# Kernel tuning notes

Measured on AMD Instinct MI355X. Metric: run time of the kernel, lower is better.

The kernel has to match this reference:

```python
import jax, jax.numpy as jnp
import numpy as np

B, S, T = 128, 1024, 512
VOCAB, E, HE, HD, ATT = 1000, 128, 64, 66, 32


def setup_inputs() -> dict:
    key = jax.random.key(0)
    ks = jax.random.split(key, 14)
    p = lambda k, shape: (jax.random.normal(k, shape, dtype=jnp.float32) * 0.05)
    return {
        'x': jax.random.randint(ks[0], (B, S), 0, VOCAB, dtype=jnp.int32),
        'c': jax.random.normal(ks[1], (B, T), dtype=jnp.float32),
        'emb': p(ks[2], (VOCAB, E)),
        'enc_Wih': p(ks[3], (4 * HE, E)),
        'enc_Whh': p(ks[4], (4 * HE, HE)),
        'enc_b': p(ks[5], (4 * HE,)),
        'att_fc_W': p(ks[6], (HE, E)),
        'att_fc_b': p(ks[7], (HE,)),
        'att_w_W': p(ks[8], (ATT, HE)),
        'att_w_b': p(ks[9], (ATT,)),
        'dec_Wih': p(ks[10], (4 * HD, ATT)),
        'dec_Whh': p(ks[11], (4 * HD, HD)),
        'dec_b': p(ks[12], (4 * HD,)),
        'fin_W': p(ks[13], (E, HD)),
        'fin_b': jnp.zeros((E,), dtype=jnp.float32),
    }


def _lstm_seq(xs, W_ih, W_hh, b, H):
    # xs: [B, S, in]; PyTorch gate order i, f, g, o
    bsz = xs.shape[0]
    gx = jnp.einsum('bsi,gi->bsg', xs, W_ih) + b  # [B,S,4H]

    def step(carry, g_t):
        h, c = carry
        g = g_t + h @ W_hh.T
        i, f, gg, o = jnp.split(g, 4, axis=-1)
        c = jax.nn.sigmoid(f) * c + jax.nn.sigmoid(i) * jnp.tanh(gg)
        h = jax.nn.sigmoid(o) * jnp.tanh(c)
        return (h, c), h

    h0 = jnp.zeros((bsz, H), xs.dtype)
    (_, _), hs = jax.lax.scan(step, (h0, h0), jnp.swapaxes(gx, 0, 1))
    return jnp.swapaxes(hs, 0, 1)  # [B,S,H]


def reference(x, c, emb, enc_Wih, enc_Whh, enc_b, att_fc_W, att_fc_b,
              att_w_W, att_w_b, dec_Wih, dec_Whh, dec_b, fin_W, fin_b):
    # encoder: embed + LSTM, returns full sequence of hidden states [B,S,64]
    enc = _lstm_seq(emb[x], enc_Wih, enc_Whh, enc_b, HE)
    bsz, steps = x.shape[0], c.shape[1]
    # initial decoder input: embedding of token 0, broadcast over batch
    x0 = jnp.broadcast_to(emb[0], (bsz, E))
    h0 = jnp.zeros((bsz, HD), enc.dtype)

    def step(carry, _):
        xemb, h, cc = carry
        # attend(a=xemb, A=enc)
        a = xemb @ att_fc_W.T + att_fc_b                     # [B,64]
        A = a[:, None, :] * enc                              # [B,S,64]
        alpha = jax.nn.softmax(
            jnp.tanh(jnp.einsum('bse,ae->bsa', A, att_w_W) + att_w_b),
            axis=-1)                                         # [B,S,32]
        beta = alpha.sum(axis=1)                             # [B,32]
        # decoder LSTM cell (one timestep)
        g = beta @ dec_Wih.T + h @ dec_Whh.T + dec_b
        i, f, gg, o = jnp.split(g, 4, axis=-1)
        cc = jax.nn.sigmoid(f) * cc + jax.nn.sigmoid(i) * jnp.tanh(gg)
        h = jax.nn.sigmoid(o) * jnp.tanh(cc)
        xemb = h @ fin_W.T + fin_b                           # feed back via final_fc
        return (xemb, h, cc), h

    _, hs = jax.lax.scan(step, (x0, h0, h0), None, length=steps)
    return jnp.swapaxes(hs, 0, 1)  # [B,T,66]
```

## Files before the change

### kernel.cpp

```cpp
#include <hip/hip_runtime.h>
#include <hip/hip_bf16.h>

#define kB 128
#define kS 1024
#define kT 512
#define kV 1000
#define kE 128
#define kHE 64
#define kHD 66
#define kATT 32
#define kGE 256
#define kGD 264

typedef __attribute__((ext_vector_type(4))) float f32x4;
typedef __attribute__((ext_vector_type(8))) short bf16x8;
typedef __attribute__((ext_vector_type(8))) unsigned short u16x8;

__device__ __forceinline__ unsigned short f2bf(float f) {
  unsigned int u = __builtin_bit_cast(unsigned int, f);
  u += 0x7FFFu + ((u >> 16) & 1u);
  return (unsigned short)(u >> 16);
}
__device__ __forceinline__ float rcp_(float x) { return __builtin_amdgcn_rcpf(x); }
__device__ __forceinline__ float fsig(float x)  { return rcp_(1.0f + __expf(-x)); }
__device__ __forceinline__ float ftanh(float x) { return 1.0f - 2.0f * rcp_(1.0f + __expf(2.0f * x)); }
__device__ __forceinline__ float fexp2(float z) {
#if __has_builtin(__builtin_amdgcn_exp2f)
  return __builtin_amdgcn_exp2f(z);
#else
  return __expf(z * 0.6931471805599453f);
#endif
}
__device__ __forceinline__ const unsigned short* launder_us(const unsigned short* p) {
  asm volatile("" : "+s"(p));
  return p;
}
__device__ __forceinline__ float dpp_red16(float v) {
  int x = __builtin_bit_cast(int, v);
  v += __builtin_bit_cast(float, __builtin_amdgcn_update_dpp(0, x, 0xB1, 0xf, 0xf, true));
  x = __builtin_bit_cast(int, v);
  v += __builtin_bit_cast(float, __builtin_amdgcn_update_dpp(0, x, 0x4E, 0xf, 0xf, true));
  x = __builtin_bit_cast(int, v);
  v += __builtin_bit_cast(float, __builtin_amdgcn_update_dpp(0, x, 0x124, 0xf, 0xf, true));
  x = __builtin_bit_cast(int, v);
  v += __builtin_bit_cast(float, __builtin_amdgcn_update_dpp(0, x, 0x128, 0xf, 0xf, true));
  return v;
}
#define DPPB(v, ctrl) __builtin_bit_cast(float, __builtin_amdgcn_update_dpp(0, __builtin_bit_cast(int, (v)), (ctrl), 0xf, 0xf, true))

__global__ __launch_bounds__(256) void prep_kernel(
    const float* __restrict__ emb, const float* __restrict__ enc_Wih,
    const float* __restrict__ enc_b, const float* __restrict__ enc_Whh,
    const float* __restrict__ att_fc_W, const float* __restrict__ att_fc_b,
    const float* __restrict__ att_w_W,
    const float* __restrict__ fin_W, const float* __restrict__ fin_b,
    const float* __restrict__ dec_Wih, const float* __restrict__ dec_Whh,
    const float* __restrict__ dec_b,
    float* __restrict__ embW, unsigned short* __restrict__ decF,
    unsigned short* __restrict__ encF, unsigned short* __restrict__ afF,
    float* __restrict__ wregF, float* __restrict__ dbias,
    float* __restrict__ wh64, float* __restrict__ wh65,
    float* __restrict__ abias, float* __restrict__ ainit) {
  int bid = blockIdx.x, tid = threadIdx.x;
  if (bid < kV) {
    float acc = enc_b[tid];
    const float* er = emb + bid * kE;
    const float* wr = enc_Wih + tid * kE;
    for (int e = 0; e < kE; ++e) acc += er[e] * wr[e];
    embW[bid * kGE + tid] = acc;
  } else if (bid == kV) {
    for (int i = tid; i < 17 * 3 * 64 * 8; i += 256) {
      int jj = i & 7, lane = (i >> 3) & 63, ts = i >> 9;
      int tile = ts / 3, ks = ts - tile * 3;
      int jp = tile * 16 + (lane & 15);
      int cell = jp >> 2, gate = jp & 3;
      int k = ks * 32 + ((lane >> 4) << 3) + jj;
      float v = 0.f;
      if (cell < kHD) {
        int j = gate * kHD + cell;
        if (k < 32) v = dec_Wih[j * kATT + k];
        else v = dec_Whh[j * kHD + (k - 32)];
      }
      decF[i] = f2bf(v);
    }
  } else if (bid == kV + 1) {
    for (int i = tid; i < 16 * 2 * 64 * 8; i += 256) {
      int jj = i & 7, lane = (i >> 3) & 63, ts = i >> 9;
      int tile = ts >> 1, ks = ts & 1;
      int j = tile * 16 + (lane & 15);
      int k = ks * 32 + ((lane >> 4) << 3) + jj;
      encF[i] = f2bf(enc_Whh[j * kHE + k]);
    }
  } else if (bid == kV + 2) {
    for (int i = tid; i < 4 * 3 * 64 * 8; i += 256) {
      int jj = i & 7, lane = (i >> 3) & 63, ts = i >> 9;
      int tile = ts / 3, ks = ts - tile * 3;
      int aidx = tile * 16 + (lane & 15);
      int m = ks * 32 + ((lane >> 4) << 3) + jj;
      float v = 0.f;
      if (m < kHD)
        for (int e = 0; e < kE; ++e) v += att_fc_W[aidx * kE + e] * fin_W[e * kHD + m];
      afF[i] = f2bf(v);
    }
  } else if (bid == kV + 3) {
    for (int i = tid; i < 8 * 64 * 4; i += 256) {
      int c = i & 3, lane = (i >> 2) & 63, jq = i >> 8;
      int half = jq & 1, kc = (jq >> 1) & 1, mt = jq >> 2;
      wregF[i] = att_w_W[(mt * 16 + (lane & 15)) * kHE + kc * 32 + ((lane >> 4) << 3) + half * 4 + c];
    }
  } else if (bid == kV + 4) {
    for (int jp = tid; jp < kGD; jp += 256) {
      int cell = jp >> 2, gate = jp & 3;
      int j = gate * kHD + cell;
      float s = 0.f;
      for (int m = 0; m < kATT; ++m) s += dec_Wih[j * kATT + m];
      dbias[jp] = dec_b[j] + 32.0f * s;
      wh64[jp] = dec_Whh[j * kHD + 64];
      wh65[jp] = dec_Whh[j * kHD + 65];
    }
  } else {
    if (tid < kHE) {
      float acc = att_fc_b[tid];
      for (int e = 0; e < kE; ++e) acc += att_fc_W[tid * kE + e] * fin_b[e];
      abias[tid] = acc;
    } else if (tid < 2 * kHE) {
      int a = tid - kHE;
      float acc = att_fc_b[a];
      for (int e = 0; e < kE; ++e) acc += emb[e] * att_fc_W[a * kE + e];
      ainit[a] = acc;
    }
  }
}

__global__ __launch_bounds__(256)
__attribute__((amdgpu_waves_per_eu(1, 1)))
void enc_kernel(
    const int* __restrict__ x, const float* __restrict__ embW,
    const unsigned short* __restrict__ encF, float* __restrict__ out) {
  __shared__ struct __align__(16) {
    unsigned short xe[64];
    float gbuf[kGE];
    int toks[kS];
  } sm;
  const int b = blockIdx.x, t = threadIdx.x, lane = t & 63, wv = t >> 6;

  for (int i = t; i < kS; i += 256) sm.toks[i] = x[b * kS + i];
  if (t < 64) sm.xe[t] = 0;

  u16x8 eQ[4][2];
  #pragma unroll
  for (int q = 0; q < 4; ++q)
    #pragma unroll
    for (int ks = 0; ks < 2; ++ks)
      eQ[q][ks] = *(const u16x8*)&encF[(((wv * 4 + q) * 2 + ks) * 64 + lane) * 8];
  __syncthreads();

  float gx0 = 0, gx1 = 0, gx2 = 0, gx3 = 0;
  if (lane < 16) {
    int tok = sm.toks[0];
    gx0 = embW[tok * kGE + wv * 64 + 0 + lane];
    gx1 = embW[tok * kGE + wv * 64 + 16 + lane];
    gx2 = embW[tok * kGE + wv * 64 + 32 + lane];
    gx3 = embW[tok * kGE + wv * 64 + 48 + lane];
  }
  float cE = 0.0f;
  unsigned short* eg = (unsigned short*)(out + (size_t)b * (kT * kHD));

  for (int s = 0; s < kS; ++s) {
    union { u16x8 u; bf16x8 v; } xa0, xa1;
    xa0.u = *(const u16x8*)&sm.xe[(lane >> 4) << 3];
    xa1.u = *(const u16x8*)&sm.xe[32 + ((lane >> 4) << 3)];
    float gn0 = 0, gn1 = 0, gn2 = 0, gn3 = 0;
    int tokn = sm.toks[(s + 1 < kS) ? (s + 1) : s];
    if (lane < 16) {
      gn0 = embW[tokn * kGE + wv * 64 + 0 + lane];
      gn1 = embW[tokn * kGE + wv * 64 + 16 + lane];
      gn2 = embW[tokn * kGE + wv * 64 + 32 + lane];
      gn3 = embW[tokn * kGE + wv * 64 + 48 + lane];
    }
    f32x4 z = {0.f, 0.f, 0.f, 0.f};
    f32x4 a0 = __builtin_amdgcn_mfma_f32_16x16x32_bf16(xa0.v, eQ[0][0], z, 0, 0, 0);
    a0 = __builtin_amdgcn_mfma_f32_16x16x32_bf16(xa1.v, eQ[0][1], a0, 0, 0, 0);
    f32x4 a1 = __builtin_amdgcn_mfma_f32_16x16x32_bf16(xa0.v, eQ[1][0], z, 0, 0, 0);
    a1 = __builtin_amdgcn_mfma_f32_16x16x32_bf16(xa1.v, eQ[1][1], a1, 0, 0, 0);
    f32x4 a2 = __builtin_amdgcn_mfma_f32_16x16x32_bf16(xa0.v, eQ[2][0], z, 0, 0, 0);
    a2 = __builtin_amdgcn_mfma_f32_16x16x32_bf16(xa1.v, eQ[2][1], a2, 0, 0, 0);
    f32x4 a3 = __builtin_amdgcn_mfma_f32_16x16x32_bf16(xa0.v, eQ[3][0], z, 0, 0, 0);
    a3 = __builtin_amdgcn_mfma_f32_16x16x32_bf16(xa1.v, eQ[3][1], a3, 0, 0, 0);
    if (lane < 16) {
      sm.gbuf[wv * 64 + 0 + lane]  = a0[0] + gx0;
      sm.gbuf[wv * 64 + 16 + lane] = a1[0] + gx1;
      sm.gbuf[wv * 64 + 32 + lane] = a2[0] + gx2;
      sm.gbuf[wv * 64 + 48 + lane] = a3[0] + gx3;
    }
    __syncthreads();
    if (t < 64) {
      float gi = sm.gbuf[t], gf = sm.gbuf[64 + t], gg = sm.gbuf[128 + t], go = sm.gbuf[192 + t];
      cE = fsig(gf) * cE + fsig(gi) * ftanh(gg);
      float h = fsig(go) * ftanh(cE);
      unsigned short hb = f2bf(h);
      sm.xe[t] = hb;
      eg[s * 64 + ((((t >> 3) ^ (s & 7)) << 3) | (t & 7))] = hb;
    }
    __syncthreads();
    gx0 = gn0; gx1 = gn1; gx2 = gn2; gx3 = gn3;
  }
}

struct __align__(16) DSm {
  unsigned short enc[kS * kHE];
  float wregL[8 * 64 * 4];
  float dbL[kGD];
  float wh64L[kGD];
  float wh65L[kGD];
  float absL[64];
  float aa[64];
  float beta[32];
  unsigned short xv[2][160];
  float hh2[2][2];
};

union U8 { u16x8 u; bf16x8 v; };

__global__ __launch_bounds__(512, 2)
void dec_kernel(
    const float* __restrict__ att_w_b,
    const unsigned short* __restrict__ decF, const unsigned short* __restrict__ afF,
    const float* __restrict__ wregF_ws, const float* __restrict__ dbias_ws,
    const float* __restrict__ wh64_ws, const float* __restrict__ wh65_ws,
    const float* __restrict__ abias_ws, const float* __restrict__ ainit_ws,
    float* __restrict__ out) {
  __shared__ DSm sm;
  const int b = blockIdx.x, t = threadIdx.x, lane = t & 63, wv = t >> 6;
  const int lr = lane & 15, g = lane >> 4;

  {
    const u16x8* src = (const u16x8*)(out + (size_t)b * (kT * kHD));
    u16x8* dst = (u16x8*)sm.enc;
    #pragma unroll
    for (int i = 0; i < 16; ++i) dst[t + i * 512] = src[t + i * 512];
  }
  ((f32x4*)sm.wregL)[t] = ((const f32x4*)wregF_ws)[t];
  for (int i = t; i < kGD; i += 512) {
    sm.dbL[i] = dbias_ws[i];
    sm.wh64L[i] = wh64_ws[i];
    sm.wh65L[i] = wh65_ws[i];
  }
  if (t < 64) { sm.absL[t] = abias_ws[t]; sm.aa[t] = ainit_ws[t]; }
  if (t < 32) sm.beta[t] = 0.f;
  for (int i = t; i < 320; i += 512) ((unsigned short*)sm.xv)[i] = 0;
  if (t < 4) ((float*)sm.hh2)[t] = 0.f;

  const float bw0 = att_w_b[lr];
  const float bw1 = att_w_b[16 + lr];
  U8 aQ[3];
  if (wv < 4) {
    #pragma unroll
    for (int ks = 0; ks < 3; ++ks)
      aQ[ks].u = *(const u16x8*)&afF[((wv * 3 + ks) * 64 + lane) * 8];
  }
  float cDa = 0.0f, cDb = 0.0f, cDc = 0.0f;
  __syncthreads();

  const int sbase = wv * 128;
  const int tileA = wv, tileB = wv + 8;
  const bool has3 = (wv == 7);

  for (int step = 0; step < kT; ++step) {
    const int cb = step & 1, nb = cb ^ 1;
    U8 qa[3], qb[3], qc[3];
    {
      const f32x4* aap = (const f32x4*)sm.aa;
      const f32x4* wrl = (const f32x4*)sm.wregL;
      bf16x8 af[2][2];
      #pragma unroll
      for (int kc = 0; kc < 2; ++kc) {
        f32x4 a0v = aap[kc * 8 + g * 2];
        f32x4 a1v = aap[kc * 8 + g * 2 + 1];
        #pragma unroll
        for (int mt = 0; mt < 2; ++mt) {
          f32x4 w0 = wrl[((mt * 2 + kc) * 2 + 0) * 64 + lane];
          f32x4 w1 = wrl[((mt * 2 + kc) * 2 + 1) * 64 + lane];
          union { bf16x8 v; __hip_bfloat162 h2[4]; } tmp;
          tmp.h2[0] = __float22bfloat162_rn(make_float2(w0.x * a0v.x, w0.y * a0v.y));
          tmp.h2[1] = __float22bfloat162_rn(make_float2(w0.z * a0v.z, w0.w * a0v.w));
          tmp.h2[2] = __float22bfloat162_rn(make_float2(w1.x * a1v.x, w1.y * a1v.y));
          tmp.h2[3] = __float22bfloat162_rn(make_float2(w1.z * a1v.z, w1.w * a1v.w));
          af[mt][kc] = tmp.v;
        }
      }
      f32x4 wc0 = {bw0, bw0, bw0, bw0};
      f32x4 wc1 = {bw1, bw1, bw1, bw1};
      float betaAcc[2] = {0.f, 0.f};
      float amax = 0.0f;
      #pragma unroll
      for (int nt = 0; nt < 8; ++nt) {
        int s = sbase + nt * 16 + lr;
        int sw = s & 7;
        U8 e0, e1;
        e0.u = *(const u16x8*)&sm.enc[s * kHE + ((g ^ sw) << 3)];
        e1.u = *(const u16x8*)&sm.enc[s * kHE + (((4 + g) ^ sw) << 3)];
        f32x4 acc0 = __builtin_amdgcn_mfma_f32_16x16x32_bf16(e0.v, af[0][0], wc0, 0, 0, 0);
        acc0 = __builtin_amdgcn_mfma_f32_16x16x32_bf16(e1.v, af[0][1], acc0, 0, 0, 0);
        f32x4 acc1 = __builtin_amdgcn_mfma_f32_16x16x32_bf16(e0.v, af[1][0], wc1, 0, 0, 0);
        acc1 = __builtin_amdgcn_mfma_f32_16x16x32_bf16(e1.v, af[1][1], acc1, 0, 0, 0);
        float u0[4], u1[4];
        #pragma unroll
        for (int r = 0; r < 4; ++r) {
          float x0 = acc0[r], x1 = acc1[r];
          amax = fmaxf(amax, fmaxf(__builtin_fabsf(x0), __builtin_fabsf(x1)));
          u0[r] = fexp2(x0 * __builtin_fmaf(x0 * x0, -0.48089835f, 1.44269504f));
          u1[r] = fexp2(x1 * __builtin_fmaf(x1 * x1, -0.48089835f, 1.44269504f));
        }
        #pragma unroll
        for (int r = 0; r < 4; ++r) {
          float invd = rcp_(dpp_red16(u0[r] + u1[r]));
          betaAcc[0] += u0[r] * invd;
          betaAcc[1] += u1[r] * invd;
        }
      }
      if (__builtin_expect(__any(amax > 0.35f), 0)) {
        betaAcc[0] = 0.f; betaAcc[1] = 0.f;
        for (int nt = 0; nt < 8; ++nt) {
          int s = sbase + nt * 16 + lr;
          int sw = s & 7;
          U8 e0, e1;
          e0.u = *(const u16x8*)&sm.enc[s * kHE + ((g ^ sw) << 3)];
          e1.u = *(const u16x8*)&sm.enc[s * kHE + (((4 + g) ^ sw) << 3)];
          f32x4 acc0 = __builtin_amdgcn_mfma_f32_16x16x32_bf16(e0.v, af[0][0], wc0, 0, 0, 0);
          acc0 = __builtin_amdgcn_mfma_f32_16x16x32_bf16(e1.v, af[0][1], acc0, 0, 0, 0);
          f32x4 acc1 = __builtin_amdgcn_mfma_f32_16x16x32_bf16(e0.v, af[1][0], wc1, 0, 0, 0);
          acc1 = __builtin_amdgcn_mfma_f32_16x16x32_bf16(e1.v, af[1][1], acc1, 0, 0, 0);
          float u0[4], u1[4];
          for (int r = 0; r < 4; ++r) {
            u0[r] = __expf(tanhf(acc0[r]));
            u1[r] = __expf(tanhf(acc1[r]));
          }
          for (int r = 0; r < 4; ++r) {
            float invd = rcp_(dpp_red16(u0[r] + u1[r]));
            betaAcc[0] += u0[r] * invd;
            betaAcc[1] += u1[r] * invd;
          }
        }
      }
      {
        const unsigned short* dFp = launder_us(decF);
        #pragma unroll
        for (int ks = 0; ks < 3; ++ks) {
          qa[ks].u = *(const u16x8*)&dFp[((tileA * 3 + ks) * 64 + lane) * 8];
          qb[ks].u = *(const u16x8*)&dFp[((tileB * 3 + ks) * 64 + lane) * 8];
        }
        if (has3) {
          #pragma unroll
          for (int ks = 0; ks < 3; ++ks)
            qc[ks].u = *(const u16x8*)&dFp[((16 * 3 + ks) * 64 + lane) * 8];
        }
      }
      #pragma unroll
      for (int mt = 0; mt < 2; ++mt) {
        float v = betaAcc[mt];
        v += __shfl_xor(v, 16);
        v += __shfl_xor(v, 32);
        if (lane < 16) atomicAdd(&sm.beta[mt * 16 + lane], v);
      }
    }
    __syncthreads();
    {
      const f32x4* pb = (const f32x4*)sm.beta;
      f32x4 b0 = pb[g * 2], b1 = pb[g * 2 + 1];
      union { bf16x8 v; __hip_bfloat162 h2[4]; } bfr;
      bfr.h2[0] = __float22bfloat162_rn(make_float2(b0.x - 32.f, b0.y - 32.f));
      bfr.h2[1] = __float22bfloat162_rn(make_float2(b0.z - 32.f, b0.w - 32.f));
      bfr.h2[2] = __float22bfloat162_rn(make_float2(b1.x - 32.f, b1.y - 32.f));
      bfr.h2[3] = __float22bfloat162_rn(make_float2(b1.z - 32.f, b1.w - 32.f));
      U8 xg1, xg2;
      xg1.u = *(const u16x8*)&sm.xv[cb][32 + (g << 3)];
      xg2.u = *(const u16x8*)&sm.xv[cb][64 + (g << 3)];
      float hh0 = sm.hh2[cb][0], hh1 = sm.hh2[cb][1];
      float* op = out + ((size_t)b * kT + step) * kHD;
      const int gate = lane & 3;
      const float kk = (gate == 2) ? 2.0f : 1.0f;
      f32x4 z = {0.f, 0.f, 0.f, 0.f};
      {
        f32x4 ga = __builtin_amdgcn_mfma_f32_16x16x32_bf16(bfr.v, qa[0].v, z, 0, 0, 0);
        ga = __builtin_amdgcn_mfma_f32_16x16x32_bf16(xg1.v, qa[1].v, ga, 0, 0, 0);
        ga = __builtin_amdgcn_mfma_f32_16x16x32_bf16(xg2.v, qa[2].v, ga, 0, 0, 0);
        int jp = tileA * 16 + lr;
        float xg = ga[0] + sm.dbL[jp] + sm.wh64L[jp] * hh0 + sm.wh65L[jp] * hh1;
        float y = fsig(kk * xg);
        float v = (gate == 2) ? (2.0f * y - 1.0f) : y;
        float q0 = DPPB(v, 0x00), q1 = DPPB(v, 0x55), q2 = DPPB(v, 0xAA), q3 = DPPB(v, 0xFF);
        float cn = q1 * cDa + q0 * q2;
        cDa = cn;
        float h = q3 * ftanh(cn);
        if (gate == 0 && lane < 16) {
          int cell = jp >> 2;
          sm.xv[nb][32 + cell] = f2bf(h);
          op[cell] = h;
        }
      }
      {
        f32x4 gb = __builtin_amdgcn_mfma_f32_16x16x32_bf16(bfr.v, qb[0].v, z, 0, 0, 0);
        gb = __builtin_amdgcn_mfma_f32_16x16x32_bf16(xg1.v, qb[1].v, gb, 0, 0, 0);
        gb = __builtin_amdgcn_mfma_f32_16x16x32_bf16(xg2.v, qb[2].v, gb, 0, 0, 0);
        int jp = tileB * 16 + lr;
        float xg = gb[0] + sm.dbL[jp] + sm.wh64L[jp] * hh0 + sm.wh65L[jp] * hh1;
        float y = fsig(kk * xg);
        float v = (gate == 2) ? (2.0f * y - 1.0f) : y;
        float q0 = DPPB(v, 0x00), q1 = DPPB(v, 0x55), q2 = DPPB(v, 0xAA), q3 = DPPB(v, 0xFF);
        float cn = q1 * cDb + q0 * q2;
        cDb = cn;
        float h = q3 * ftanh(cn);
        if (gate == 0 && lane < 16) {
          int cell = jp >> 2;
          sm.xv[nb][32 + cell] = f2bf(h);
          op[cell] = h;
        }
      }
      if (has3) {
        f32x4 gc = __builtin_amdgcn_mfma_f32_16x16x32_bf16(bfr.v, qc[0].v, z, 0, 0, 0);
        gc = __builtin_amdgcn_mfma_f32_16x16x32_bf16(xg1.v, qc[1].v, gc, 0, 0, 0);
        gc = __builtin_amdgcn_mfma_f32_16x16x32_bf16(xg2.v, qc[2].v, gc, 0, 0, 0);
        int jp = 256 + (lane & 7);
        float xg = gc[0] + sm.dbL[jp] + sm.wh64L[jp] * hh0 + sm.wh65L[jp] * hh1;
        float y = fsig(kk * xg);
        float v = (gate == 2) ? (2.0f * y - 1.0f) : y;
        float q0 = DPPB(v, 0x00), q1 = DPPB(v, 0x55), q2 = DPPB(v, 0xAA), q3 = DPPB(v, 0xFF);
        float cn = q1 * cDc + q0 * q2;
        cDc = cn;
        float h = q3 * ftanh(cn);
        if (gate == 0 && lane < 8) {
          int cell = 64 + (lane >> 2);
          sm.xv[nb][32 + cell] = f2bf(h);
          sm.hh2[nb][lane >> 2] = h;
          op[cell] = h;
        }
      }
    }
    __syncthreads();
    if (wv < 4) {
      U8 y0, y1, y2;
      y0.u = *(const u16x8*)&sm.xv[nb][32 + (g << 3)];
      y1.u = *(const u16x8*)&sm.xv[nb][64 + (g << 3)];
      y2.u = *(const u16x8*)&sm.xv[nb][96 + (g << 3)];
      f32x4 z = {0.f, 0.f, 0.f, 0.f};
      f32x4 acc = __builtin_amdgcn_mfma_f32_16x16x32_bf16(y0.v, aQ[0].v, z, 0, 0, 0);
      acc = __builtin_amdgcn_mfma_f32_16x16x32_bf16(y1.v, aQ[1].v, acc, 0, 0, 0);
      acc = __builtin_amdgcn_mfma_f32_16x16x32_bf16(y2.v, aQ[2].v, acc, 0, 0, 0);
      if (lane < 16) sm.aa[wv * 16 + lane] = acc[0] + sm.absL[wv * 16 + lane];
    } else if (wv == 4) {
      if (lane < 32) sm.beta[lane] = 0.f;
    }
    __syncthreads();
  }
}

extern "C" void kernel_launch(void* const* d_in, const int* in_sizes, int n_in,
                              void* d_out, int out_size, void* d_ws, size_t ws_size,
                              hipStream_t stream) {
  const int*   x        = (const int*)d_in[0];
  const float* emb      = (const float*)d_in[2];
  const float* enc_Wih  = (const float*)d_in[3];
  const float* enc_Whh  = (const float*)d_in[4];
  const float* enc_b    = (const float*)d_in[5];
  const float* att_fc_W = (const float*)d_in[6];
  const float* att_fc_b = (const float*)d_in[7];
  const float* att_w_W  = (const float*)d_in[8];
  const float* att_w_b  = (const float*)d_in[9];
  const float* dec_Wih  = (const float*)d_in[10];
  const float* dec_Whh  = (const float*)d_in[11];
  const float* dec_b    = (const float*)d_in[12];
  const float* fin_W    = (const float*)d_in[13];
  const float* fin_b    = (const float*)d_in[14];
  float* out = (float*)d_out;

  float* embW = (float*)d_ws;
  unsigned short* decF = (unsigned short*)(embW + kV * kGE);
  unsigned short* encF = decF + 17 * 3 * 64 * 8;
  unsigned short* afF  = encF + 16 * 2 * 64 * 8;
  float* wregF = (float*)(afF + 4 * 3 * 64 * 8);
  float* dbias = wregF + 8 * 64 * 4;
  float* wh64  = dbias + kGD;
  float* wh65  = wh64 + kGD;
  float* abias = wh65 + kGD;
  float* ainit = abias + kHE;

  prep_kernel<<<dim3(kV + 6), dim3(256), 0, stream>>>(
      emb, enc_Wih, enc_b, enc_Whh, att_fc_W, att_fc_b, att_w_W, fin_W, fin_b,
      dec_Wih, dec_Whh, dec_b, embW, decF, encF, afF, wregF, dbias, wh64, wh65,
      abias, ainit);
  enc_kernel<<<dim3(kB), dim3(256), 0, stream>>>(x, embW, encF, out);
  dec_kernel<<<dim3(kB), dim3(512), 0, stream>>>(
      att_w_b, decF, afF, wregF, dbias, wh64, wh65, abias, ainit, out);
}
```

Measured before the change: 2.886 ms.

## Replicate attention-fc compute per wave to remove a barrier and beta atomics

Each of the 8 waves now recomputes the full 64-wide attention fc projection into its own private aa buffer, with the fc weights staged in LDS. This removes the final __syncthreads of every decoder step. Beta partials are written per wave and summed by the reader instead of accumulated with LDS atomicAdd, which also removes the per-step beta zeroing. In exchange each wave does 4x the MFMA and LDS reads for the fc step, and LDS use grows, which could lower occupancy.

```diff
diff --git a/kernel.cpp b/kernel.cpp
--- a/kernel.cpp
+++ b/kernel.cpp
@@ -210,12 +210,13 @@
 struct __align__(16) DSm {
   unsigned short enc[kS * kHE];
   float wregL[8 * 64 * 4];
+  unsigned short afL[4 * 3 * 64 * 8];
   float dbL[kGD];
   float wh64L[kGD];
   float wh65L[kGD];
   float absL[64];
-  float aa[64];
-  float beta[32];
+  float aaW[8][64];
+  float betaW[8][32];
   unsigned short xv[2][160];
   float hh2[2][2];
 };
@@ -241,24 +242,19 @@
     for (int i = 0; i < 16; ++i) dst[t + i * 512] = src[t + i * 512];
   }
   ((f32x4*)sm.wregL)[t] = ((const f32x4*)wregF_ws)[t];
+  for (int i = t; i < 768; i += 512) ((u16x8*)sm.afL)[i] = ((const u16x8*)afF)[i];
   for (int i = t; i < kGD; i += 512) {
     sm.dbL[i] = dbias_ws[i];
     sm.wh64L[i] = wh64_ws[i];
     sm.wh65L[i] = wh65_ws[i];
   }
-  if (t < 64) { sm.absL[t] = abias_ws[t]; sm.aa[t] = ainit_ws[t]; }
-  if (t < 32) sm.beta[t] = 0.f;
+  if (t < 64) sm.absL[t] = abias_ws[t];
+  sm.aaW[t >> 6][t & 63] = ainit_ws[t & 63];
   for (int i = t; i < 320; i += 512) ((unsigned short*)sm.xv)[i] = 0;
   if (t < 4) ((float*)sm.hh2)[t] = 0.f;
 
   const float bw0 = att_w_b[lr];
   const float bw1 = att_w_b[16 + lr];
-  U8 aQ[3];
-  if (wv < 4) {
-    #pragma unroll
-    for (int ks = 0; ks < 3; ++ks)
-      aQ[ks].u = *(const u16x8*)&afF[((wv * 3 + ks) * 64 + lane) * 8];
-  }
   float cDa = 0.0f, cDb = 0.0f, cDc = 0.0f;
   __syncthreads();
 
@@ -270,7 +266,7 @@
     const int cb = step & 1, nb = cb ^ 1;
     U8 qa[3], qb[3], qc[3];
     {
-      const f32x4* aap = (const f32x4*)sm.aa;
+      const f32x4* aap = (const f32x4*)sm.aaW[wv];
       const f32x4* wrl = (const f32x4*)sm.wregL;
       bf16x8 af[2][2];
       #pragma unroll
@@ -361,13 +357,18 @@
         float v = betaAcc[mt];
         v += __shfl_xor(v, 16);
         v += __shfl_xor(v, 32);
-        if (lane < 16) atomicAdd(&sm.beta[mt * 16 + lane], v);
+        if (lane < 16) sm.betaW[wv][mt * 16 + lane] = v;
       }
     }
     __syncthreads();
     {
-      const f32x4* pb = (const f32x4*)sm.beta;
-      f32x4 b0 = pb[g * 2], b1 = pb[g * 2 + 1];
+      const f32x4* bwp = (const f32x4*)sm.betaW;
+      f32x4 b0 = bwp[g * 2], b1 = bwp[g * 2 + 1];
+      #pragma unroll
+      for (int w = 1; w < 8; ++w) {
+        b0 += bwp[w * 8 + g * 2];
+        b1 += bwp[w * 8 + g * 2 + 1];
+      }
       union { bf16x8 v; __hip_bfloat162 h2[4]; } bfr;
       bfr.h2[0] = __float22bfloat162_rn(make_float2(b0.x - 32.f, b0.y - 32.f));
       bfr.h2[1] = __float22bfloat162_rn(make_float2(b0.z - 32.f, b0.w - 32.f));
@@ -438,20 +439,24 @@
       }
     }
     __syncthreads();
-    if (wv < 4) {
+    {
       U8 y0, y1, y2;
       y0.u = *(const u16x8*)&sm.xv[nb][32 + (g << 3)];
       y1.u = *(const u16x8*)&sm.xv[nb][64 + (g << 3)];
       y2.u = *(const u16x8*)&sm.xv[nb][96 + (g << 3)];
       f32x4 z = {0.f, 0.f, 0.f, 0.f};
-      f32x4 acc = __builtin_amdgcn_mfma_f32_16x16x32_bf16(y0.v, aQ[0].v, z, 0, 0, 0);
-      acc = __builtin_amdgcn_mfma_f32_16x16x32_bf16(y1.v, aQ[1].v, acc, 0, 0, 0);
-      acc = __builtin_amdgcn_mfma_f32_16x16x32_bf16(y2.v, aQ[2].v, acc, 0, 0, 0);
-      if (lane < 16) sm.aa[wv * 16 + lane] = acc[0] + sm.absL[wv * 16 + lane];
-    } else if (wv == 4) {
-      if (lane < 32) sm.beta[lane] = 0.f;
-    }
-    __syncthreads();
+      #pragma unroll
+      for (int tt = 0; tt < 4; ++tt) {
+        U8 f0, f1, f2;
+        f0.u = *(const u16x8*)&sm.afL[((tt * 3 + 0) * 64 + lane) * 8];
+        f1.u = *(const u16x8*)&sm.afL[((tt * 3 + 1) * 64 + lane) * 8];
+        f2.u = *(const u16x8*)&sm.afL[((tt * 3 + 2) * 64 + lane) * 8];
+        f32x4 acc = __builtin_amdgcn_mfma_f32_16x16x32_bf16(y0.v, f0.v, z, 0, 0, 0);
+        acc = __builtin_amdgcn_mfma_f32_16x16x32_bf16(y1.v, f1.v, acc, 0, 0, 0);
+        acc = __builtin_amdgcn_mfma_f32_16x16x32_bf16(y2.v, f2.v, acc, 0, 0, 0);
+        if (lane < 16) sm.aaW[wv][tt * 16 + lane] = acc[0] + sm.absL[tt * 16 + lane];
+      }
+    }
   }
 }
 
```

After: 3.119 ms. +8.1%, slower.
